# Optimization experiments

Measured on AMD Instinct MI355X. Metric: run time of the kernel, lower is better.

The kernel has to match this reference:

```python
import jax, jax.numpy as jnp
import numpy as np

N_GENES = 20000   # adj_shape[0], source nodes
N_DRUGS = 4000    # adj_shape[1], target nodes
IN_C = 1024
OUT_C = 512
N_EDGES = 262144


def setup_inputs() -> dict:
    key = jax.random.key(0)
    k1, k2, k3 = jax.random.split(key, 3)
    x = jax.random.normal(k1, (N_GENES, IN_C), dtype=jnp.float32)
    # glorot-uniform init as in utils.glorot
    limit = np.sqrt(6.0 / (IN_C + OUT_C)).astype(np.float32)
    weight = jax.random.uniform(k2, (IN_C, OUT_C), dtype=jnp.float32,
                                minval=-limit, maxval=limit)
    bias = jnp.zeros((OUT_C,), dtype=jnp.float32)
    edge_index = jax.random.randint(k3, (2, N_EDGES), 0, N_DRUGS, dtype=jnp.int64)
    return {"x": x, "weight": weight, "bias": bias, "edge_index": edge_index}


def reference(x, weight, bias, edge_index):
    """BipartiteGCN.forward: out = (D_r^-1/2 A D_c^-1/2)^T (x W) + b.

    A is the (n_genes, n_drugs) bipartite adjacency built from edge_index
    (row0 = gene/source ids, row1 = drug/target ids); duplicate edges are
    summed (scipy csr semantics), which edge-wise accumulation reproduces.
    """
    src = edge_index[0]  # gene ids, index rows of A
    dst = edge_index[1]  # drug ids, index cols of A
    ones = jnp.ones((src.shape[0],), dtype=jnp.float32)
    row_deg = jax.ops.segment_sum(ones, src, num_segments=N_GENES)   # rowsum
    col_deg = jax.ops.segment_sum(ones, dst, num_segments=N_DRUGS)   # colsum
    inv_sqrt_row = jnp.where(row_deg > 0, jax.lax.rsqrt(row_deg), 0.0)
    inv_sqrt_col = jnp.where(col_deg > 0, jax.lax.rsqrt(col_deg), 0.0)
    coef = inv_sqrt_row[src] * inv_sqrt_col[dst]                      # [E]

    xw = x @ weight                                                   # [n_genes, out_c]
    msg = xw[src] * coef[:, None]                                     # gather + scale, [E, out_c]
    out = jax.ops.segment_sum(msg, dst, num_segments=N_DRUGS)         # scatter-add, [n_drugs, out_c]
    return out + bias
```

## Files before the change

kernel.cpp:

```cpp
#include <hip/hip_runtime.h>
#include <hip/hip_bf16.h>

#define N_GENES 20000
#define N_DRUGS 4000
#define IN_C 1024
#define OUT_C 512
#define N_EDGES 262144
#define NB 64
#define EPB 4096
#define RS 24064

typedef __attribute__((ext_vector_type(8))) short short8;
typedef __attribute__((ext_vector_type(4))) float f32x4;
typedef __attribute__((ext_vector_type(4))) unsigned short us4;
typedef __attribute__((ext_vector_type(8))) unsigned short us8;

__device__ __forceinline__ float b2f(unsigned short u) {
    union { unsigned int i; float f; } v;
    v.i = ((unsigned int)u) << 16;
    return v.f;
}

__device__ __forceinline__ unsigned short f2b(float f) {
    union { float f; unsigned int i; } v;
    v.f = f;
    unsigned int x = v.i;
    return (unsigned short)((x + 0x7fffu + ((x >> 16) & 1u)) >> 16);
}

__device__ __forceinline__ void gld16(const void* g, void* l) {
    __builtin_amdgcn_global_load_lds((const __attribute__((address_space(1))) unsigned int*)g,
                                     (__attribute__((address_space(3))) unsigned int*)l,
                                     16, 0, 0);
}

__global__ __launch_bounds__(256) void k_hist(const int* __restrict__ ei,
                                              const float* __restrict__ w,
                                              int* __restrict__ part,
                                              unsigned short* __restrict__ wt) {
    __shared__ int hd[4000];
    __shared__ int hs[10048];
    __shared__ float tile[32][36];
    int t = threadIdx.x;
    if (blockIdx.x < NB) {
        int b = blockIdx.x, e0 = b * EPB;
        for (int i = t; i < 4000; i += 256) hd[i] = 0;
        for (int i = t; i < 10000; i += 256) hs[i] = 0;
        __syncthreads();
        for (int i = t; i < EPB; i += 256) {
            int s = ei[e0 + i];
            int d = ei[N_EDGES + e0 + i];
            atomicAdd(&hd[d], 1);
            if (s < 10000) atomicAdd(&hs[s], 1);
        }
        __syncthreads();
        int* pr = part + b * RS;
        for (int i = t; i < 4000; i += 256) pr[i] = hd[i];
        for (int i = t; i < 10000; i += 256) pr[4000 + i] = hs[i];
        __syncthreads();
        for (int i = t; i < 10000; i += 256) hs[i] = 0;
        __syncthreads();
        for (int i = t; i < EPB; i += 256) {
            int s = ei[e0 + i];
            if (s >= 10000) atomicAdd(&hs[s - 10000], 1);
        }
        __syncthreads();
        for (int i = t; i < 10000; i += 256) pr[14000 + i] = hs[i];
    } else {
        int idx = blockIdx.x - NB;
        int bk = (idx & 31) * 32;
        int bn = (idx >> 5) * 32;
        int row = t >> 3, col = (t & 7) * 4;
        f32x4 vv = *(const f32x4*)&w[(size_t)(bk + row) * OUT_C + bn + col];
        tile[row][col + 0] = vv[0];
        tile[row][col + 1] = vv[1];
        tile[row][col + 2] = vv[2];
        tile[row][col + 3] = vv[3];
        __syncthreads();
        int n = t >> 3, kc = (t & 7) * 4;
        us4 o;
#pragma unroll
        for (int j = 0; j < 4; j++) o[j] = f2b(tile[kc + j][n]);
        *(us4*)&wt[(size_t)(bn + n) * IN_C + bk + kc] = o;
    }
}

__global__ __launch_bounds__(256) void k_prep(const int* __restrict__ part,
                                              int* __restrict__ part_off,
                                              float* __restrict__ inv_src,
                                              float* __restrict__ inv_dst,
                                              int* __restrict__ grpflag,
                                              int* __restrict__ bstart) {
    __shared__ int sdeg[4000];
    __shared__ int wsum[4];
    int t = threadIdx.x, blk = blockIdx.x;
    if (blk < 16) {
        int d = blk * 256 + t;
        if (d < N_DRUGS) {
            int run = 0;
            for (int b = 0; b < NB; b++) {
                int v = part[b * RS + d];
                part_off[b * 4000 + d] = run;
                run += v;
            }
            inv_dst[d] = (run > 0) ? rsqrtf((float)run) : 0.0f;
        }
    } else if (blk < 95) {
        int g = (blk - 16) * 256 + t;
        int run = 0;
        if (g < N_GENES)
            for (int b = 0; b < NB; b++) run += part[b * RS + 4000 + g];
        bool act = (g < N_GENES) && (run > 0);
        if (g < N_GENES) inv_src[g] = act ? rsqrtf((float)run) : 0.0f;
        unsigned long long m = __ballot(act);
        if ((t & 63) == 0) grpflag[g >> 6] = (m != 0ull) ? 1 : 0;
    } else {
        for (int k = 0; k < 16; k++) {
            int d = t + k * 256;
            if (d < N_DRUGS) {
                int run = 0;
                for (int b = 0; b < NB; b++) run += part[b * RS + d];
                sdeg[d] = run;
            }
        }
        __syncthreads();
        int lane = t & 63, wv = t >> 6;
        int v[16];
        int sum = 0;
#pragma unroll
        for (int j = 0; j < 16; j++) {
            int idx = t * 16 + j;
            int dv = (idx < N_DRUGS) ? sdeg[idx] : 0;
            v[j] = sum;
            sum += dv;
        }
        int s = sum;
        for (int off = 1; off < 64; off <<= 1) {
            int u = __shfl_up(s, off, 64);
            if (lane >= off) s += u;
        }
        if (lane == 63) wsum[wv] = s;
        __syncthreads();
        int wbase = 0;
        for (int k2 = 0; k2 < wv; k2++) wbase += wsum[k2];
        int base = wbase + s - sum;
#pragma unroll
        for (int j = 0; j < 16; j++) {
            int idx = t * 16 + j;
            if (idx < N_DRUGS) bstart[idx] = base + v[j];
        }
        if (t == 255) bstart[N_DRUGS] = wbase + s;
    }
}

__global__ __launch_bounds__(256) void k_sx(const int* __restrict__ ei,
                                            const float* __restrict__ x,
                                            const int* __restrict__ part_off,
                                            const int* __restrict__ bstart,
                                            const float* __restrict__ inv_src,
                                            int* __restrict__ eslot,
                                            unsigned short* __restrict__ xa) {
    __shared__ int off[4000];
    __shared__ int h2[4000];
    int t = threadIdx.x;
    if (blockIdx.x < NB) {
        int b = blockIdx.x, e0 = b * EPB;
        for (int i = t; i < 4000; i += 256) {
            off[i] = bstart[i] + part_off[b * 4000 + i];
            h2[i] = 0;
        }
        __syncthreads();
        for (int i = t; i < EPB; i += 256) {
            int s = ei[e0 + i];
            int d = ei[N_EDGES + e0 + i];
            int r = atomicAdd(&h2[d], 1);
            eslot[off[d] + r] = s;
        }
    } else {
        for (int g = (int)blockIdx.x - NB; g < N_GENES; g += 1024) {
            float c = inv_src[g];
            if (c == 0.0f) continue;
            const float* src = x + (size_t)g * IN_C;
            f32x4 v = *(const f32x4*)&src[t * 4];
            us4 o;
            o[0] = f2b(v[0] * c); o[1] = f2b(v[1] * c);
            o[2] = f2b(v[2] * c); o[3] = f2b(v[3] * c);
            *(us4*)&xa[(size_t)g * IN_C + t * 4] = o;
        }
    }
}

__global__ __launch_bounds__(256) void k_gemm(const unsigned short* __restrict__ xa,
                                              const unsigned short* __restrict__ wt,
                                              const int* __restrict__ grpflag,
                                              unsigned short* __restrict__ xw) {
    __shared__ unsigned short As[2][4096];
    __shared__ unsigned short Bs[2][4096];
    if (!grpflag[blockIdx.x]) return;
    int bm = blockIdx.x * 64;
    int bn = blockIdx.y * 64;
    int t = threadIdx.x, lane = t & 63, wave = t >> 6;
    int wr = wave >> 1, wc = wave & 1;
    int fr = lane & 15, kq = lane >> 4;

    int r0 = t >> 3;
    int csrc = ((t & 7) ^ (r0 & 7)) * 8;
    const unsigned short* ga = xa + (size_t)(bm + r0) * IN_C + csrc;
    const unsigned short* gb = wt + (size_t)(bn + r0) * IN_C + csrc;

    int arow = wr * 32 + fr;
    int aof0 = arow * 64 + ((kq ^ (arow & 7)) * 8);
    int aof1 = arow * 64 + (((kq + 4) ^ (arow & 7)) * 8);
    int brow = wc * 32 + fr;
    int bof0 = brow * 64 + ((kq ^ (brow & 7)) * 8);
    int bof1 = brow * 64 + (((kq + 4) ^ (brow & 7)) * 8);

    f32x4 acc[2][2] = {};

    {
        unsigned short* la = &As[0][0] + wave * 512;
        unsigned short* lb = &Bs[0][0] + wave * 512;
        gld16(ga, la);              gld16(ga + 32 * IN_C, la + 2048);
        gld16(gb, lb);              gld16(gb + 32 * IN_C, lb + 2048);
    }
    asm volatile("s_waitcnt vmcnt(0)" ::: "memory");
    __syncthreads();

    const int NK = IN_C / 64;
    for (int ki = 0; ki < NK; ki++) {
        int buf = ki & 1;
        if (ki + 1 < NK) {
            int k0 = (ki + 1) * 64;
            unsigned short* la = &As[buf ^ 1][0] + wave * 512;
            unsigned short* lb = &Bs[buf ^ 1][0] + wave * 512;
            gld16(ga + k0, la);              gld16(ga + k0 + 32 * IN_C, la + 2048);
            gld16(gb + k0, lb);              gld16(gb + k0 + 32 * IN_C, lb + 2048);
        }
        const unsigned short* A = As[buf];
        const unsigned short* B = Bs[buf];
        short8 a0 = *(const short8*)&A[aof0];
        short8 a1 = *(const short8*)&A[aof0 + 1024];
        short8 b0 = *(const short8*)&B[bof0];
        short8 b1 = *(const short8*)&B[bof0 + 1024];
        acc[0][0] = __builtin_amdgcn_mfma_f32_16x16x32_bf16(a0, b0, acc[0][0], 0, 0, 0);
        acc[0][1] = __builtin_amdgcn_mfma_f32_16x16x32_bf16(a0, b1, acc[0][1], 0, 0, 0);
        acc[1][0] = __builtin_amdgcn_mfma_f32_16x16x32_bf16(a1, b0, acc[1][0], 0, 0, 0);
        acc[1][1] = __builtin_amdgcn_mfma_f32_16x16x32_bf16(a1, b1, acc[1][1], 0, 0, 0);
        a0 = *(const short8*)&A[aof1];
        a1 = *(const short8*)&A[aof1 + 1024];
        b0 = *(const short8*)&B[bof1];
        b1 = *(const short8*)&B[bof1 + 1024];
        acc[0][0] = __builtin_amdgcn_mfma_f32_16x16x32_bf16(a0, b0, acc[0][0], 0, 0, 0);
        acc[0][1] = __builtin_amdgcn_mfma_f32_16x16x32_bf16(a0, b1, acc[0][1], 0, 0, 0);
        acc[1][0] = __builtin_amdgcn_mfma_f32_16x16x32_bf16(a1, b0, acc[1][0], 0, 0, 0);
        acc[1][1] = __builtin_amdgcn_mfma_f32_16x16x32_bf16(a1, b1, acc[1][1], 0, 0, 0);
        asm volatile("s_waitcnt vmcnt(0)" ::: "memory");
        __syncthreads();
    }

    int fq = lane >> 4;
#pragma unroll
    for (int mi = 0; mi < 2; mi++)
#pragma unroll
        for (int ni = 0; ni < 2; ni++)
#pragma unroll
            for (int j = 0; j < 4; j++) {
                int row = bm + wr * 32 + mi * 16 + fq * 4 + j;
                int col = bn + wc * 32 + ni * 16 + fr;
                xw[(size_t)row * OUT_C + col] = f2b(acc[mi][ni][j]);
            }
}

__global__ __launch_bounds__(256) void k_aggregate(const unsigned short* __restrict__ xw,
                                                   const int* __restrict__ eslot,
                                                   const int* __restrict__ bstart,
                                                   const float* __restrict__ inv_dst,
                                                   const float* __restrict__ bias,
                                                   float* __restrict__ out) {
    int wave = threadIdx.x >> 6, lane = threadIdx.x & 63;
    int d = blockIdx.x * 4 + wave;
    if (d >= N_DRUGS) return;

    float acc[8] = {0.f, 0.f, 0.f, 0.f, 0.f, 0.f, 0.f, 0.f};
    int s0 = bstart[d], s1 = bstart[d + 1];
    const unsigned short* xw_l = xw + lane * 8;

    int b = s0;
    for (; b + 64 <= s1; b += 64) {
        int idx = eslot[b + lane];
#pragma unroll 4
        for (int j = 0; j < 64; j++) {
            int r = __shfl(idx, j);
            us8 v = *(const us8*)&xw_l[(size_t)r * OUT_C];
#pragma unroll
            for (int k = 0; k < 8; k++) acc[k] += b2f(v[k]);
        }
    }
    int rem = s1 - b;
    if (rem > 0) {
        int idx = (lane < rem) ? eslot[b + lane] : 0;
        for (int j = 0; j < rem; j++) {
            int r = __shfl(idx, j);
            us8 v = *(const us8*)&xw_l[(size_t)r * OUT_C];
#pragma unroll
            for (int k = 0; k < 8; k++) acc[k] += b2f(v[k]);
        }
    }

    float wd = inv_dst[d];
    f32x4 b0 = *(const f32x4*)&bias[lane * 8];
    f32x4 b1 = *(const f32x4*)&bias[lane * 8 + 4];
    f32x4 o0, o1;
#pragma unroll
    for (int k = 0; k < 4; k++) { o0[k] = acc[k] * wd + b0[k]; o1[k] = acc[k + 4] * wd + b1[k]; }
    float* op = out + (size_t)d * OUT_C + lane * 8;
    *(f32x4*)op = o0;
    *(f32x4*)(op + 4) = o1;
}

extern "C" void kernel_launch(void* const* d_in, const int* in_sizes, int n_in,
                              void* d_out, int out_size, void* d_ws, size_t ws_size,
                              hipStream_t stream) {
    const float* x    = (const float*)d_in[0];
    const float* w    = (const float*)d_in[1];
    const float* bias = (const float*)d_in[2];
    const int*   ei   = (const int*)d_in[3];
    float*       out  = (float*)d_out;

    char* ws = (char*)d_ws;
    int*   part     = (int*)(ws + 0);
    int*   part_off = (int*)(ws + 6160384);
    float* inv_src  = (float*)(ws + 7184384);
    float* inv_dst  = (float*)(ws + 7264512);
    int*   bstart   = (int*)(ws + 7280640);
    int*   grpflag  = (int*)(ws + 7296768);
    int*   eslot    = (int*)(ws + 7298048);
    unsigned short* wt = (unsigned short*)(ws + 8346624);
    unsigned short* xa = (unsigned short*)(ws + 9395200);
    unsigned short* xw = (unsigned short*)(ws + 50420736);

    k_hist<<<NB + 512, 256, 0, stream>>>(ei, w, part, wt);
    k_prep<<<96, 256, 0, stream>>>(part, part_off, inv_src, inv_dst, grpflag, bstart);
    k_sx<<<NB + 1024, 256, 0, stream>>>(ei, x, part_off, bstart, inv_src, eslot, xa);
    dim3 gg((N_GENES + 63) / 64, OUT_C / 64);
    k_gemm<<<gg, 256, 0, stream>>>(xa, wt, grpflag, xw);
    k_aggregate<<<(N_DRUGS + 3) / 4, 256, 0, stream>>>(xw, eslot, bstart, inv_dst, bias, out);
}
```

Before: 188.9 us.

## Split degree prep into LDS-staged reduction kernel and separate single-block scan

The degree-prep kernel now stages each 64x256 slice of per-block histograms into shared memory with vectorized int4 loads before summing, replacing strided scalar global loads. The single serial block that recomputed all drug degrees and ran the prefix scan is removed. Drug degrees are written to a new buffer and scanned by a separate one-block kernel. The histogram row stride is padded so the int4 loads stay in bounds. This trades one extra kernel launch for removing the long serial tail block.

```diff
diff --git a/kernel.cpp b/kernel.cpp
--- a/kernel.cpp
+++ b/kernel.cpp
@@ -8,7 +8,7 @@
 #define N_EDGES 262144
 #define NB 64
 #define EPB 4096
-#define RS 24064
+#define RS 24256
 
 typedef __attribute__((ext_vector_type(8))) short short8;
 typedef __attribute__((ext_vector_type(4))) float f32x4;
@@ -54,7 +54,7 @@
             if (s < 10000) atomicAdd(&hs[s], 1);
         }
         __syncthreads();
-        int* pr = part + b * RS;
+        int* pr = part + (size_t)b * RS;
         for (int i = t; i < 4000; i += 256) pr[i] = hd[i];
         for (int i = t; i < 10000; i += 256) pr[4000 + i] = hs[i];
         __syncthreads();
@@ -85,72 +85,88 @@
     }
 }
 
-__global__ __launch_bounds__(256) void k_prep(const int* __restrict__ part,
-                                              int* __restrict__ part_off,
-                                              float* __restrict__ inv_src,
-                                              float* __restrict__ inv_dst,
-                                              int* __restrict__ grpflag,
-                                              int* __restrict__ bstart) {
-    __shared__ int sdeg[4000];
-    __shared__ int wsum[4];
-    int t = threadIdx.x, blk = blockIdx.x;
-    if (blk < 16) {
-        int d = blk * 256 + t;
+__global__ __launch_bounds__(256) void k_prep1(const int* __restrict__ part,
+                                               int* __restrict__ part_off,
+                                               int* __restrict__ sdeg,
+                                               float* __restrict__ inv_src,
+                                               float* __restrict__ inv_dst,
+                                               int* __restrict__ grpflag) {
+    __shared__ int sm[64][256];
+    int t = threadIdx.x;
+    int rq = t >> 6;
+    int c4 = (t & 63) * 4;
+    if (blockIdx.x < 16) {
+        int d0 = blockIdx.x * 256;
+#pragma unroll
+        for (int p = 0; p < 16; p++) {
+            int b = p * 4 + rq;
+            int4 v = *(const int4*)&part[(size_t)b * RS + d0 + c4];
+            sm[b][c4 + 0] = v.x; sm[b][c4 + 1] = v.y;
+            sm[b][c4 + 2] = v.z; sm[b][c4 + 3] = v.w;
+        }
+        __syncthreads();
+        int d = d0 + t;
         if (d < N_DRUGS) {
             int run = 0;
-            for (int b = 0; b < NB; b++) {
-                int v = part[b * RS + d];
+#pragma unroll
+            for (int b = 0; b < 64; b++) {
                 part_off[b * 4000 + d] = run;
-                run += v;
+                run += sm[b][t];
             }
+            sdeg[d] = run;
             inv_dst[d] = (run > 0) ? rsqrtf((float)run) : 0.0f;
         }
-    } else if (blk < 95) {
-        int g = (blk - 16) * 256 + t;
+    } else {
+        int g0 = (blockIdx.x - 16) * 256;
+#pragma unroll
+        for (int p = 0; p < 16; p++) {
+            int b = p * 4 + rq;
+            int4 v = *(const int4*)&part[(size_t)b * RS + 4000 + g0 + c4];
+            sm[b][c4 + 0] = v.x; sm[b][c4 + 1] = v.y;
+            sm[b][c4 + 2] = v.z; sm[b][c4 + 3] = v.w;
+        }
+        __syncthreads();
+        int g = g0 + t;
         int run = 0;
-        if (g < N_GENES)
-            for (int b = 0; b < NB; b++) run += part[b * RS + 4000 + g];
+#pragma unroll
+        for (int b = 0; b < 64; b++) run += sm[b][t];
         bool act = (g < N_GENES) && (run > 0);
         if (g < N_GENES) inv_src[g] = act ? rsqrtf((float)run) : 0.0f;
         unsigned long long m = __ballot(act);
         if ((t & 63) == 0) grpflag[g >> 6] = (m != 0ull) ? 1 : 0;
-    } else {
-        for (int k = 0; k < 16; k++) {
-            int d = t + k * 256;
-            if (d < N_DRUGS) {
-                int run = 0;
-                for (int b = 0; b < NB; b++) run += part[b * RS + d];
-                sdeg[d] = run;
-            }
-        }
-        __syncthreads();
-        int lane = t & 63, wv = t >> 6;
-        int v[16];
-        int sum = 0;
-#pragma unroll
-        for (int j = 0; j < 16; j++) {
-            int idx = t * 16 + j;
-            int dv = (idx < N_DRUGS) ? sdeg[idx] : 0;
-            v[j] = sum;
-            sum += dv;
-        }
-        int s = sum;
-        for (int off = 1; off < 64; off <<= 1) {
-            int u = __shfl_up(s, off, 64);
-            if (lane >= off) s += u;
-        }
-        if (lane == 63) wsum[wv] = s;
-        __syncthreads();
-        int wbase = 0;
-        for (int k2 = 0; k2 < wv; k2++) wbase += wsum[k2];
-        int base = wbase + s - sum;
-#pragma unroll
-        for (int j = 0; j < 16; j++) {
-            int idx = t * 16 + j;
-            if (idx < N_DRUGS) bstart[idx] = base + v[j];
-        }
-        if (t == 255) bstart[N_DRUGS] = wbase + s;
-    }
+    }
+}
+
+__global__ __launch_bounds__(256) void k_scan(const int* __restrict__ sdeg,
+                                              int* __restrict__ bstart) {
+    __shared__ int wsum[4];
+    int t = threadIdx.x;
+    int lane = t & 63, wv = t >> 6;
+    int v[16];
+    int sum = 0;
+#pragma unroll
+    for (int j = 0; j < 16; j++) {
+        int idx = t * 16 + j;
+        int d = (idx < N_DRUGS) ? sdeg[idx] : 0;
+        v[j] = sum;
+        sum += d;
+    }
+    int s = sum;
+    for (int off = 1; off < 64; off <<= 1) {
+        int u = __shfl_up(s, off, 64);
+        if (lane >= off) s += u;
+    }
+    if (lane == 63) wsum[wv] = s;
+    __syncthreads();
+    int wbase = 0;
+    for (int k = 0; k < wv; k++) wbase += wsum[k];
+    int base = wbase + s - sum;
+#pragma unroll
+    for (int j = 0; j < 16; j++) {
+        int idx = t * 16 + j;
+        if (idx < N_DRUGS) bstart[idx] = base + v[j];
+    }
+    if (t == 255) bstart[N_DRUGS] = wbase + s;
 }
 
 __global__ __launch_bounds__(256) void k_sx(const int* __restrict__ ei,
@@ -329,18 +345,20 @@
 
     char* ws = (char*)d_ws;
     int*   part     = (int*)(ws + 0);
-    int*   part_off = (int*)(ws + 6160384);
-    float* inv_src  = (float*)(ws + 7184384);
-    float* inv_dst  = (float*)(ws + 7264512);
-    int*   bstart   = (int*)(ws + 7280640);
-    int*   grpflag  = (int*)(ws + 7296768);
-    int*   eslot    = (int*)(ws + 7298048);
-    unsigned short* wt = (unsigned short*)(ws + 8346624);
-    unsigned short* xa = (unsigned short*)(ws + 9395200);
-    unsigned short* xw = (unsigned short*)(ws + 50420736);
+    int*   part_off = (int*)(ws + 6209536);
+    int*   sdeg     = (int*)(ws + 7233536);
+    float* inv_src  = (float*)(ws + 7249920);
+    float* inv_dst  = (float*)(ws + 7330048);
+    int*   bstart   = (int*)(ws + 7346176);
+    int*   grpflag  = (int*)(ws + 7362304);
+    int*   eslot    = (int*)(ws + 7363584);
+    unsigned short* wt = (unsigned short*)(ws + 8412160);
+    unsigned short* xa = (unsigned short*)(ws + 9460736);
+    unsigned short* xw = (unsigned short*)(ws + 50486272);
 
     k_hist<<<NB + 512, 256, 0, stream>>>(ei, w, part, wt);
-    k_prep<<<96, 256, 0, stream>>>(part, part_off, inv_src, inv_dst, grpflag, bstart);
+    k_prep1<<<95, 256, 0, stream>>>(part, part_off, sdeg, inv_src, inv_dst, grpflag);
+    k_scan<<<1, 256, 0, stream>>>(sdeg, bstart);
     k_sx<<<NB + 1024, 256, 0, stream>>>(ei, x, part_off, bstart, inv_src, eslot, xa);
     dim3 gg((N_GENES + 63) / 64, OUT_C / 64);
     k_gemm<<<gg, 256, 0, stream>>>(xa, wt, grpflag, xw);
```

After: 182.7 us. 1.03x faster.
